# Kernel tuning notes

Hardware: AMD Instinct MI355X
Metric: run time of the kernel (lower is better)

Reference implementation:

```python
import jax, jax.numpy as jnp
import numpy as np

B, T, TS, J, D, H = 4, 512, 512, 17, 256, 8
CD = D // H
SCALE = CD ** -0.5


def setup_inputs() -> dict:
    key = jax.random.key(0)
    ks = jax.random.split(key, 7)
    return {
        "q": jax.random.normal(ks[0], (B, T, J, D), dtype=jnp.float32),
        "kv": jax.random.normal(ks[1], (B, TS, J, D), dtype=jnp.float32),
        "Wq": jax.random.normal(ks[2], (D, D), dtype=jnp.float32) * (D ** -0.5),
        "Wk": jax.random.normal(ks[3], (D, D), dtype=jnp.float32) * (D ** -0.5),
        "Wv": jax.random.normal(ks[4], (D, D), dtype=jnp.float32) * (D ** -0.5),
        "Wp": jax.random.normal(ks[5], (D, D), dtype=jnp.float32) * (D ** -0.5),
        "bp": jnp.zeros((D,), dtype=jnp.float32),
    }


def reference(q, kv, Wq, Wk, Wv, Wp, bp):
    b, t, j, d = q.shape
    t_sup = kv.shape[1]
    h, cd = H, CD
    # linear projections (torch Linear: x @ W^T), split heads -> [b,h,j,t,cd]
    qh = (q @ Wq.T).reshape(b, t, j, h, cd).transpose(0, 3, 2, 1, 4)
    kh = (kv @ Wk.T).reshape(b, t_sup, j, h, cd).transpose(0, 3, 2, 1, 4)
    vh = (kv @ Wv.T).reshape(b, t_sup, j, h, cd).transpose(0, 3, 2, 1, 4)
    # full attention matrix over temporal axes: [b,h,j,t,t_sup]
    scores = jnp.einsum("bhjtc,bhjsc->bhjts", qh, kh) * SCALE
    attn = jax.nn.softmax(scores, axis=-1)
    out = jnp.einsum("bhjts,bhjsc->bhjtc", attn, vh)
    out = out.transpose(0, 3, 2, 1, 4).reshape(b, t, j, d)  # [b,t,j,d]
    return out @ Wp.T + bp
```

## Files before the change

kernel.cpp:

```cpp
#include <hip/hip_runtime.h>
#include <hip/hip_bf16.h>

#define BB 4
#define TT 512
#define JJ 17
#define DD 256
#define HH 8
#define MROWS (BB*TT*JJ)
#define SZE ((size_t)MROWS * DD)
#define WSZ (DD*DD)
#define QSCALE 0.2550265247510319f
#define RST (17*256)

typedef short v8s __attribute__((ext_vector_type(8)));
typedef float v4f __attribute__((ext_vector_type(4)));

__device__ __forceinline__ unsigned short f2bf(float f) {
    union { float f; unsigned int u; } c; c.f = f;
    unsigned int u = c.u;
    return (unsigned short)((u + 0x7FFF + ((u >> 16) & 1)) >> 16);
}
__device__ __forceinline__ unsigned int pkbf(float lo, float hi) {
    union { float f; unsigned int u; } a, b; a.f = lo; b.f = hi;
    return __builtin_amdgcn_perm(b.u + 0x8000u, a.u + 0x8000u, 0x07060302u);
}
__device__ __forceinline__ float fexp2(float x) {
    return __builtin_amdgcn_exp2f(x);
}

__device__ __forceinline__ void gld16(const unsigned short* g, unsigned short* l) {
    __builtin_amdgcn_global_load_lds(
        (const __attribute__((address_space(1))) void*)g,
        (__attribute__((address_space(3))) void*)l,
        16, 0, 0);
}

__global__ __launch_bounds__(256) void prepw_kernel(
    const float* __restrict__ Wq, const float* __restrict__ Wk,
    const float* __restrict__ Wv, const float* __restrict__ Wp,
    unsigned short* __restrict__ Wqb, unsigned short* __restrict__ Wkb,
    unsigned short* __restrict__ Wvb, unsigned short* __restrict__ Wpb)
{
    size_t k = ((size_t)blockIdx.x * 256 + threadIdx.x) * 8;
    int w = (int)(k >> 16);
    size_t off = k & (WSZ - 1);
    const float* src = (w == 0) ? Wq : (w == 1) ? Wk : (w == 2) ? Wv : Wp;
    unsigned short* dst = (w == 0) ? Wqb : (w == 1) ? Wkb : (w == 2) ? Wvb : Wpb;
    float4 x0 = *(const float4*)(src + off);
    float4 x1 = *(const float4*)(src + off + 4);
    union { unsigned short s[8]; int4 v; } u;
    u.s[0] = f2bf(x0.x); u.s[1] = f2bf(x0.y);
    u.s[2] = f2bf(x0.z); u.s[3] = f2bf(x0.w);
    u.s[4] = f2bf(x1.x); u.s[5] = f2bf(x1.y);
    u.s[6] = f2bf(x1.z); u.s[7] = f2bf(x1.w);
    *(int4*)(dst + off) = u.v;
}

__global__ __launch_bounds__(512) void gemm_kernel(
    const float* __restrict__ Aq,
    const float* __restrict__ Akv,
    const unsigned short* __restrict__ W0,
    const unsigned short* __restrict__ W1,
    const unsigned short* __restrict__ W2,
    unsigned short* __restrict__ Y0,
    unsigned short* __restrict__ Y1,
    unsigned short* __restrict__ Y2)
{
    const int z = blockIdx.y;
    const float* A          = (z == 0) ? Aq : Akv;
    const float ascale      = (z == 0) ? QSCALE : 1.f;
    const unsigned short* W = (z == 0) ? W0 : (z == 1) ? W1 : W2;
    unsigned short* Y       = (z == 0) ? Y0 : (z == 1) ? Y1 : Y2;

    const int bm = blockIdx.x;

    __shared__ unsigned short As[2][128 * 32];
    __shared__ unsigned short Bs[2][256 * 32];

    const int tid  = threadIdx.x;
    const int wv   = tid >> 6;
    const int lane = tid & 63;
    const int wm   = wv & 1;
    const int wn   = wv >> 1;
    const int quad = lane >> 4;
    const int l16  = lane & 15;

    const int srow  = tid >> 2;
    const int chunk = tid & 3;
    const int s4    = srow & 15;
    const int cg    = chunk ^ ((s4 ^ (s4 >> 2)) & 3);
    const float* gA = A + (size_t)(bm * 128 + srow) * 256 + cg * 8;
    const unsigned short* gB0 = W + (size_t)srow * 256 + cg * 8;
    const unsigned short* gB1 = W + (size_t)(128 + srow) * 256 + cg * 8;
    unsigned short* lA  = &As[0][tid * 8];
    unsigned short* lB0 = &Bs[0][tid * 8];
    unsigned short* lB1 = &Bs[0][4096 + tid * 8];

    const int rch8 = (quad ^ ((l16 ^ (l16 >> 2)) & 3)) * 8;

    v4f acc[4][4] = {};

    {
        float4 a0 = *(const float4*)(gA);
        float4 a1 = *(const float4*)(gA + 4);
        union { unsigned short s[8]; int4 v; } ua;
        ua.s[0] = f2bf(a0.x * ascale); ua.s[1] = f2bf(a0.y * ascale);
        ua.s[2] = f2bf(a0.z * ascale); ua.s[3] = f2bf(a0.w * ascale);
        ua.s[4] = f2bf(a1.x * ascale); ua.s[5] = f2bf(a1.y * ascale);
        ua.s[6] = f2bf(a1.z * ascale); ua.s[7] = f2bf(a1.w * ascale);
        *(int4*)(lA) = ua.v;
    }
    gld16(gB0, lB0);
    gld16(gB1, lB1);
    __syncthreads();

    for (int kt = 0; kt < 8; ++kt) {
        const int cur = kt & 1;
        const int nb  = cur ^ 1;
        float4 a0, a1;
        if (kt < 7) {
            const int nk = (kt + 1) * 32;
            a0 = *(const float4*)(gA + nk);
            a1 = *(const float4*)(gA + nk + 4);
            gld16(gB0 + nk, lB0 + nb * 8192);
            gld16(gB1 + nk, lB1 + nb * 8192);
        }
        v8s a[4], b[4];
        #pragma unroll
        for (int i = 0; i < 4; ++i)
            a[i] = *(const v8s*)(&As[cur][(wm * 64 + i * 16 + l16) * 32 + rch8]);
        #pragma unroll
        for (int j = 0; j < 4; ++j)
            b[j] = *(const v8s*)(&Bs[cur][(wn * 64 + j * 16 + l16) * 32 + rch8]);
        #pragma unroll
        for (int i = 0; i < 4; ++i)
            #pragma unroll
            for (int j = 0; j < 4; ++j)
                acc[i][j] = __builtin_amdgcn_mfma_f32_16x16x32_bf16(
                    a[i], b[j], acc[i][j], 0, 0, 0);
        if (kt < 7) {
            union { unsigned short s[8]; int4 v; } ua;
            ua.s[0] = f2bf(a0.x * ascale); ua.s[1] = f2bf(a0.y * ascale);
            ua.s[2] = f2bf(a0.z * ascale); ua.s[3] = f2bf(a0.w * ascale);
            ua.s[4] = f2bf(a1.x * ascale); ua.s[5] = f2bf(a1.y * ascale);
            ua.s[6] = f2bf(a1.z * ascale); ua.s[7] = f2bf(a1.w * ascale);
            *(int4*)(lA + nb * 4096) = ua.v;
        }
        __syncthreads();
    }

    #pragma unroll
    for (int i = 0; i < 4; ++i)
        #pragma unroll
        for (int j = 0; j < 4; ++j)
            #pragma unroll
            for (int r = 0; r < 4; ++r) {
                int gm = bm * 128 + wm * 64 + i * 16 + quad * 4 + r;
                int gn = wn * 64 + j * 16 + l16;
                Y[(size_t)gm * 256 + gn] = f2bf(acc[i][j][r]);
            }
}

__global__ __launch_bounds__(256) void gemmo_kernel(
    const unsigned short* __restrict__ A,
    const unsigned short* __restrict__ W,
    const float* __restrict__ bias,
    float* __restrict__ out)
{
    const int bm = blockIdx.x;

    __shared__ unsigned short As[2][64 * 32];
    __shared__ unsigned short Bs[2][256 * 32];

    const int tid  = threadIdx.x;
    const int lane = tid & 63;
    const int wn   = tid >> 6;
    const int quad = lane >> 4;
    const int l16  = lane & 15;

    const int arow  = tid >> 2;
    const int chunk = tid & 3;
    const int cgA   = (chunk ^ ((arow ^ (arow >> 2)) & 3)) * 8;
    const unsigned short* gA = A + (size_t)(bm * 64 + arow) * 256 + cgA;
    const unsigned short* gB = W + (size_t)arow * 256 + cgA;
    unsigned short* lA = &As[0][tid * 8];
    unsigned short* lB = &Bs[0][tid * 8];

    const int rch8 = (quad ^ ((l16 ^ (l16 >> 2)) & 3)) * 8;

    v4f acc[4][4] = {};

    gld16(gA, lA);
    #pragma unroll
    for (int p = 0; p < 4; ++p)
        gld16(gB + (size_t)p * 64 * 256, lB + p * 2048);
    __syncthreads();

    for (int kt = 0; kt < 8; ++kt) {
        const int cur = kt & 1;
        if (kt < 7) {
            const int nk = (kt + 1) * 32;
            const int nb = cur ^ 1;
            gld16(gA + nk, lA + nb * 2048);
            #pragma unroll
            for (int p = 0; p < 4; ++p)
                gld16(gB + (size_t)p * 64 * 256 + nk, lB + nb * 8192 + p * 2048);
        }
        v8s a[4], b[4];
        #pragma unroll
        for (int i = 0; i < 4; ++i)
            a[i] = *(const v8s*)(&As[cur][(i * 16 + l16) * 32 + rch8]);
        #pragma unroll
        for (int j = 0; j < 4; ++j)
            b[j] = *(const v8s*)(&Bs[cur][(wn * 64 + j * 16 + l16) * 32 + rch8]);
        #pragma unroll
        for (int i = 0; i < 4; ++i)
            #pragma unroll
            for (int j = 0; j < 4; ++j)
                acc[i][j] = __builtin_amdgcn_mfma_f32_16x16x32_bf16(
                    a[i], b[j], acc[i][j], 0, 0, 0);
        __syncthreads();
    }

    #pragma unroll
    for (int i = 0; i < 4; ++i)
        #pragma unroll
        for (int j = 0; j < 4; ++j)
            #pragma unroll
            for (int r = 0; r < 4; ++r) {
                int gm = bm * 64 + i * 16 + quad * 4 + r;
                int gn = wn * 64 + j * 16 + l16;
                out[(size_t)gm * 256 + gn] = acc[i][j][r] + bias[gn];
            }
}

#define VST 136
#define PST 72

__global__ __launch_bounds__(256) void attn_kernel(
    const unsigned short* __restrict__ Qp,
    const unsigned short* __restrict__ Kp,
    const unsigned short* __restrict__ Vp,
    unsigned short* __restrict__ Att)
{
    const int id  = blockIdx.x;
    const int bjh = (id & 7) | ((id >> 5) << 3);
    const int qt  = (id >> 3) & 3;
    const int h   = bjh & 7;
    const int bj  = bjh >> 3;
    const int j   = bj % 17;
    const int b_  = bj / 17;

    __shared__ unsigned short Ks[128 * 40];
    __shared__ unsigned short Vs[32 * VST];
    __shared__ unsigned short Ps[128 * PST];
    __shared__ float Ls[128];

    const int tid  = threadIdx.x;
    const int wave = tid >> 6;
    const int lane = tid & 63;
    const int quad = lane >> 4;
    const int l16  = lane & 15;

    const int base0 = b_ * 512 * RST + j * 256 + h * 32;

    v8s qa[2];
    #pragma unroll
    for (int fi = 0; fi < 2; ++fi)
        qa[fi] = *(const v8s*)(
            Qp + base0 + (qt * 128 + wave * 32 + fi * 16 + l16) * RST + quad * 8);

    float lacc[2] = {0.f, 0.f};
    v4f accO[2][2] = {};

    for (int kc = 0; kc < 4; ++kc) {
        __syncthreads();
        #pragma unroll
        for (int c = 0; c < 2; ++c) {
            int krow = wave * 16 + l16 + c * 64;
            *(int4*)(&Ks[krow * 40 + quad * 8]) = *(const int4*)(
                Kp + base0 + (kc * 128 + krow) * RST + quad * 8);
        }
        #pragma unroll
        for (int c = 0; c < 2; ++c) {
            int idx  = c * 256 + tid;
            int srow = idx >> 2;
            int cd0  = (idx & 3) << 3;
            int xof  = (((srow >> 3) ^ (cd0 >> 3)) << 3) + (srow & 7);
            union { int4 v; unsigned short s[8]; } u;
            u.v = *(const int4*)(
                Vp + base0 + (kc * 128 + srow) * RST + cd0);
            #pragma unroll
            for (int i = 0; i < 8; ++i)
                Vs[(cd0 + i) * VST + xof] = u.s[i];
        }
        __syncthreads();

        #pragma unroll
        for (int half = 0; half < 2; ++half) {
            v4f accST[4][2] = {};
            __builtin_amdgcn_s_setprio(1);
            #pragma unroll
            for (int si = 0; si < 4; ++si) {
                v8s kb = *(const v8s*)(&Ks[((half * 4 + si) * 16 + l16) * 40 + quad * 8]);
                #pragma unroll
                for (int fi = 0; fi < 2; ++fi)
                    accST[si][fi] = __builtin_amdgcn_mfma_f32_16x16x32_bf16(
                        kb, qa[fi], accST[si][fi], 0, 0, 0);
            }
            __builtin_amdgcn_s_setprio(0);
            #pragma unroll
            for (int fi = 0; fi < 2; ++fi) {
                int prow = (wave * 32 + fi * 16 + l16) * PST;
                #pragma unroll
                for (int si = 0; si < 4; ++si) {
                    float p0 = fexp2(accST[si][fi][0]);
                    float p1 = fexp2(accST[si][fi][1]);
                    float p2 = fexp2(accST[si][fi][2]);
                    float p3 = fexp2(accST[si][fi][3]);
                    lacc[fi] += (p0 + p1) + (p2 + p3);
                    uint2 pk;
                    pk.x = pkbf(p0, p1);
                    pk.y = pkbf(p2, p3);
                    *(uint2*)(&Ps[prow + si * 16 + quad * 4]) = pk;
                }
            }
            asm volatile("s_waitcnt lgkmcnt(0)" ::: "memory");

            __builtin_amdgcn_s_setprio(1);
            #pragma unroll
            for (int ks = 0; ks < 2; ++ks) {
                v8s pa[2];
                #pragma unroll
                for (int fi = 0; fi < 2; ++fi)
                    pa[fi] = *(const v8s*)(&Ps[(wave * 32 + fi * 16 + l16) * PST +
                                               ks * 32 + quad * 8]);
                #pragma unroll
                for (int nj = 0; nj < 2; ++nj) {
                    int cd  = nj * 16 + l16;
                    int blk = (half * 8 + ks * 4 + quad) ^ (cd >> 3);
                    v8s vb = *(const v8s*)(&Vs[cd * VST + (blk << 3)]);
                    #pragma unroll
                    for (int fi = 0; fi < 2; ++fi)
                        accO[fi][nj] = __builtin_amdgcn_mfma_f32_16x16x32_bf16(
                            pa[fi], vb, accO[fi][nj], 0, 0, 0);
                }
            }
            __builtin_amdgcn_s_setprio(0);
        }
    }

    #pragma unroll
    for (int fi = 0; fi < 2; ++fi) {
        float lv = lacc[fi];
        lv += __shfl_xor(lv, 16);
        lv += __shfl_xor(lv, 32);
        if (quad == 0) Ls[wave * 32 + fi * 16 + l16] = lv;
    }
    asm volatile("s_waitcnt lgkmcnt(0)" ::: "memory");

    #pragma unroll
    for (int fi = 0; fi < 2; ++fi) {
        float4 lv = *(float4*)(&Ls[wave * 32 + fi * 16 + quad * 4]);
        float rl[4] = {1.f / lv.x, 1.f / lv.y, 1.f / lv.z, 1.f / lv.w};
        #pragma unroll
        for (int nj = 0; nj < 2; ++nj) {
            #pragma unroll
            for (int r = 0; r < 4; ++r) {
                int trow = qt * 128 + wave * 32 + fi * 16 + quad * 4 + r;
                int cd   = nj * 16 + l16;
                float v  = accO[fi][nj][r] * rl[r];
                Att[(size_t)(base0 + trow * RST + cd)] = f2bf(v);
            }
        }
    }
}

extern "C" void kernel_launch(void* const* d_in, const int* in_sizes, int n_in,
                              void* d_out, int out_size, void* d_ws, size_t ws_size,
                              hipStream_t stream) {
    const float* q  = (const float*)d_in[0];
    const float* kv = (const float*)d_in[1];
    const float* Wq = (const float*)d_in[2];
    const float* Wk = (const float*)d_in[3];
    const float* Wv = (const float*)d_in[4];
    const float* Wp = (const float*)d_in[5];
    const float* bp = (const float*)d_in[6];

    unsigned short* ws  = (unsigned short*)d_ws;
    unsigned short* Qp  = ws;
    unsigned short* Kp  = ws + SZE;
    unsigned short* Vp  = ws + 2 * SZE;
    unsigned short* Att = ws + 3 * SZE;
    unsigned short* Wqb = ws + 4 * SZE;
    unsigned short* Wkb = Wqb + WSZ;
    unsigned short* Wvb = Wkb + WSZ;
    unsigned short* Wpb = Wvb + WSZ;
    float* out = (float*)d_out;

    prepw_kernel<<<128, 256, 0, stream>>>(Wq, Wk, Wv, Wp,
                                          Wqb, Wkb, Wvb, Wpb);
    gemm_kernel<<<dim3(272, 3), 512, 0, stream>>>(
        q, kv, Wqb, Wkb, Wvb, Qp, Kp, Vp);
    attn_kernel<<<dim3(2176), 256, 0, stream>>>(Qp, Kp, Vp, Att);
    gemmo_kernel<<<dim3(544), 256, 0, stream>>>(Att, Wpb, bp, out);
}
```

Measured before the change: 202.0 us.

## Keep softmax probabilities in registers and use 32x32 MFMA for PV

The attention kernel no longer writes the exponentiated scores P to shared memory and reads them back. Lanes swap packed bf16 values across the 16-lane halves with cross-lane shuffles so that P directly forms the A operand of a 32x32x16 MFMA against V. This removes the Ps LDS buffer, its waitcnt barrier and the LDS traffic, which lowers LDS use and allows launch bounds to request 8 blocks per CU. In exchange it adds shuffle and select instructions, interleaves exp and MFMA work per 16-key slice, and the larger 16-float accumulator raises register pressure under the tighter occupancy bound.

```diff
diff --git a/kernel.cpp b/kernel.cpp
--- a/kernel.cpp
+++ b/kernel.cpp
@@ -14,6 +14,7 @@
 
 typedef short v8s __attribute__((ext_vector_type(8)));
 typedef float v4f __attribute__((ext_vector_type(4)));
+typedef float v16f __attribute__((ext_vector_type(16)));
 
 __device__ __forceinline__ unsigned short f2bf(float f) {
     union { float f; unsigned int u; } c; c.f = f;
@@ -235,9 +236,8 @@
 }
 
 #define VST 136
-#define PST 72
-
-__global__ __launch_bounds__(256) void attn_kernel(
+
+__global__ __launch_bounds__(256, 8) void attn_kernel(
     const unsigned short* __restrict__ Qp,
     const unsigned short* __restrict__ Kp,
     const unsigned short* __restrict__ Vp,
@@ -253,7 +253,6 @@
 
     __shared__ unsigned short Ks[128 * 40];
     __shared__ unsigned short Vs[32 * VST];
-    __shared__ unsigned short Ps[128 * PST];
     __shared__ float Ls[128];
 
     const int tid  = threadIdx.x;
@@ -261,6 +260,8 @@
     const int lane = tid & 63;
     const int quad = lane >> 4;
     const int l16  = lane & 15;
+    const int qo   = quad & 1;
+    const int q2   = quad >> 1;
 
     const int base0 = b_ * 512 * RST + j * 256 + h * 32;
 
@@ -271,7 +272,7 @@
             Qp + base0 + (qt * 128 + wave * 32 + fi * 16 + l16) * RST + quad * 8);
 
     float lacc[2] = {0.f, 0.f};
-    v4f accO[2][2] = {};
+    v16f accO = {};
 
     for (int kc = 0; kc < 4; ++kc) {
         __syncthreads();
@@ -298,55 +299,38 @@
 
         #pragma unroll
         for (int half = 0; half < 2; ++half) {
-            v4f accST[4][2] = {};
-            __builtin_amdgcn_s_setprio(1);
             #pragma unroll
             for (int si = 0; si < 4; ++si) {
                 v8s kb = *(const v8s*)(&Ks[((half * 4 + si) * 16 + l16) * 40 + quad * 8]);
-                #pragma unroll
-                for (int fi = 0; fi < 2; ++fi)
-                    accST[si][fi] = __builtin_amdgcn_mfma_f32_16x16x32_bf16(
-                        kb, qa[fi], accST[si][fi], 0, 0, 0);
+                v4f st0 = {}, st1 = {};
+                __builtin_amdgcn_s_setprio(1);
+                st0 = __builtin_amdgcn_mfma_f32_16x16x32_bf16(kb, qa[0], st0, 0, 0, 0);
+                st1 = __builtin_amdgcn_mfma_f32_16x16x32_bf16(kb, qa[1], st1, 0, 0, 0);
+                __builtin_amdgcn_s_setprio(0);
+                float p00 = fexp2(st0[0]), p01 = fexp2(st0[1]);
+                float p02 = fexp2(st0[2]), p03 = fexp2(st0[3]);
+                float p10 = fexp2(st1[0]), p11 = fexp2(st1[1]);
+                float p12 = fexp2(st1[2]), p13 = fexp2(st1[3]);
+                lacc[0] += (p00 + p01) + (p02 + p03);
+                lacc[1] += (p10 + p11) + (p12 + p13);
+                unsigned int D00 = pkbf(p00, p01), D01 = pkbf(p02, p03);
+                unsigned int D10 = pkbf(p10, p11), D11 = pkbf(p12, p13);
+                unsigned int P0 = qo ? D00 : D10;
+                unsigned int P1 = qo ? D01 : D11;
+                unsigned int S0 = __shfl_xor(P0, 16);
+                unsigned int S1 = __shfl_xor(P1, 16);
+                union { unsigned int u[4]; v8s v; } pa;
+                pa.u[0] = qo ? S0 : D00;
+                pa.u[1] = qo ? S1 : D01;
+                pa.u[2] = qo ? D10 : S0;
+                pa.u[3] = qo ? D11 : S1;
+                int cd   = qo * 16 + l16;
+                int sblk = half * 8 + si * 2 + q2;
+                v8s vb = *(const v8s*)(&Vs[cd * VST + ((sblk ^ (cd >> 3)) << 3)]);
+                __builtin_amdgcn_s_setprio(1);
+                accO = __builtin_amdgcn_mfma_f32_32x32x16_bf16(pa.v, vb, accO, 0, 0, 0);
+                __builtin_amdgcn_s_setprio(0);
             }
-            __builtin_amdgcn_s_setprio(0);
-            #pragma unroll
-            for (int fi = 0; fi < 2; ++fi) {
-                int prow = (wave * 32 + fi * 16 + l16) * PST;
-                #pragma unroll
-                for (int si = 0; si < 4; ++si) {
-                    float p0 = fexp2(accST[si][fi][0]);
-                    float p1 = fexp2(accST[si][fi][1]);
-                    float p2 = fexp2(accST[si][fi][2]);
-                    float p3 = fexp2(accST[si][fi][3]);
-                    lacc[fi] += (p0 + p1) + (p2 + p3);
-                    uint2 pk;
-                    pk.x = pkbf(p0, p1);
-                    pk.y = pkbf(p2, p3);
-                    *(uint2*)(&Ps[prow + si * 16 + quad * 4]) = pk;
-                }
-            }
-            asm volatile("s_waitcnt lgkmcnt(0)" ::: "memory");
-
-            __builtin_amdgcn_s_setprio(1);
-            #pragma unroll
-            for (int ks = 0; ks < 2; ++ks) {
-                v8s pa[2];
-                #pragma unroll
-                for (int fi = 0; fi < 2; ++fi)
-                    pa[fi] = *(const v8s*)(&Ps[(wave * 32 + fi * 16 + l16) * PST +
-                                               ks * 32 + quad * 8]);
-                #pragma unroll
-                for (int nj = 0; nj < 2; ++nj) {
-                    int cd  = nj * 16 + l16;
-                    int blk = (half * 8 + ks * 4 + quad) ^ (cd >> 3);
-                    v8s vb = *(const v8s*)(&Vs[cd * VST + (blk << 3)]);
-                    #pragma unroll
-                    for (int fi = 0; fi < 2; ++fi)
-                        accO[fi][nj] = __builtin_amdgcn_mfma_f32_16x16x32_bf16(
-                            pa[fi], vb, accO[fi][nj], 0, 0, 0);
-                }
-            }
-            __builtin_amdgcn_s_setprio(0);
         }
     }
 
@@ -359,19 +343,17 @@
     }
     asm volatile("s_waitcnt lgkmcnt(0)" ::: "memory");
 
-    #pragma unroll
-    for (int fi = 0; fi < 2; ++fi) {
-        float4 lv = *(float4*)(&Ls[wave * 32 + fi * 16 + quad * 4]);
+    const int cdo = qo * 16 + l16;
+    #pragma unroll
+    for (int g = 0; g < 4; ++g) {
+        float4 lv = *(float4*)(&Ls[wave * 32 + g * 8 + q2 * 4]);
         float rl[4] = {1.f / lv.x, 1.f / lv.y, 1.f / lv.z, 1.f / lv.w};
         #pragma unroll
-        for (int nj = 0; nj < 2; ++nj) {
-            #pragma unroll
-            for (int r = 0; r < 4; ++r) {
-                int trow = qt * 128 + wave * 32 + fi * 16 + quad * 4 + r;
-                int cd   = nj * 16 + l16;
-                float v  = accO[fi][nj][r] * rl[r];
-                Att[(size_t)(base0 + trow * RST + cd)] = f2bf(v);
-            }
+        for (int r = 0; r < 4; ++r) {
+            int qrow = g * 8 + q2 * 4 + r;
+            int trow = qt * 128 + wave * 32 + qrow;
+            float v  = accO[g * 4 + r] * rl[r];
+            Att[(size_t)(base0 + trow * RST + cdo)] = f2bf(v);
         }
     }
 }
```

Result: slower. 211.9 us (+4.9%).
